# Performance work log

Measured on AMD Instinct MI355X. Metric: run time of the kernel, lower is better.

The kernel has to match this reference:

```python
import jax, jax.numpy as jnp
import numpy as np

COMMITMENT_COST = 0.25


def setup_inputs() -> dict:
    key = jax.random.key(0)
    k1, k2 = jax.random.split(key)
    B, S, D, K = 16, 4096, 256, 4096
    inputs = jax.random.normal(k1, (B, S, D), dtype=jnp.float32)
    # codebook ~ embedding.weight (init scale irrelevant for correctness baseline)
    codebook = jax.random.normal(k2, (K, D), dtype=jnp.float32)
    return {"inputs": inputs, "codebook": codebook}


def reference(inputs, codebook):
    B, S, D = inputs.shape
    flat = inputs.reshape(-1, D)  # (N, D)
    distances = (
        jnp.sum(flat * flat, axis=1, keepdims=True)
        + jnp.sum(codebook * codebook, axis=1)
        - 2.0 * jnp.matmul(flat, codebook.T)
    )
    encoding_indices = jnp.argmin(distances, axis=1)  # (N,)
    quantized = codebook[encoding_indices].reshape(inputs.shape)  # gather
    # commitment loss: beta * mse(inputs, sg(quantized))
    diff = inputs - jax.lax.stop_gradient(quantized)
    commitment_loss = COMMITMENT_COST * jnp.mean(diff * diff)
    # straight-through estimator
    quantized_st = inputs + jax.lax.stop_gradient(quantized - inputs)
    return quantized_st, commitment_loss, encoding_indices
```

## Files before the change

kernel.cpp:

```cpp
#include <hip/hip_runtime.h>
#include <stdint.h>

typedef _Float16 half8 __attribute__((ext_vector_type(8)));
typedef float f32x4 __attribute__((ext_vector_type(4)));

#define DDIM 256
#define KCODES 4096
#define BM 128
#define BN 128
#define DELTA 0.02f
#define FLT_BIG 3.4e38f

#define GLOAD_LDS(gsrc, ldst)                                                        \
    __builtin_amdgcn_global_load_lds(                                                \
        (const __attribute__((address_space(1))) void*)(const void*)(gsrc),          \
        (__attribute__((address_space(3))) void*)(void*)(ldst), 16, 0, 0)

__global__ void cvt_hl_kernel(const float* __restrict__ src, half8* __restrict__ dst) {
    int gid = blockIdx.x * 256 + threadIdx.x;
    int q = gid & 3;
    int ch = (gid >> 2) & 7;
    long row = gid >> 5;
    const float* s = src + row * DDIM + ch * 32 + q * 8;
    const float4 f0 = ((const float4*)s)[0];
    const float4 f1 = ((const float4*)s)[1];
    float vv[8] = {f0.x, f0.y, f0.z, f0.w, f1.x, f1.y, f1.z, f1.w};
    half8 hi, lo;
    #pragma unroll
    for (int j = 0; j < 8; ++j) {
        float v = vv[j];
        _Float16 h = (_Float16)v;
        hi[j] = h; lo[j] = (_Float16)(v - (float)h);
    }
    half8* d = dst + ((row * 8 + ch) << 3);
    d[q] = hi;
    d[q + 4] = lo;
}

__global__ void enorm_kernel(const float* __restrict__ cb, float* __restrict__ en, int K) {
    int gid = blockIdx.x * blockDim.x + threadIdx.x;
    int code = gid >> 6;
    int lane = threadIdx.x & 63;
    if (code >= K) return;
    const float4 v = *reinterpret_cast<const float4*>(&cb[(size_t)code * DDIM + lane * 4]);
    float s = v.x * v.x + v.y * v.y + v.z * v.z + v.w * v.w;
    #pragma unroll
    for (int off = 32; off > 0; off >>= 1) s += __shfl_xor(s, off, 64);
    if (lane == 0) en[code] = s;
}

__global__ __launch_bounds__(256, 2)
void vq_mfma_kernel(const half8* x16, const half8* __restrict__ cb16,
                    const float* __restrict__ en, int* __restrict__ bidx,
                    int* __restrict__ list, int* __restrict__ counter) {
    __shared__ __align__(16) half8 Abuf[2][BM * 8];
    __shared__ __align__(16) half8 Bbuf[2][BN * 8];
    __shared__ float red_d[2][BM];
    __shared__ float red_d2[2][BM];
    __shared__ int   red_i[2][BM];

    const int tid = threadIdx.x;
    const int lane = tid & 63;
    const int w = tid >> 6;
    const int wr = w >> 1, wc = w & 1;
    const int l15 = lane & 15, l4 = lane >> 4;
    const int brow = blockIdx.x * BM;

    const int lrow = lane >> 3;
    const int swz = (lane & 7) ^ lrow;
    const half8* pA0 = x16 + (size_t)(brow + (w     ) * 8 + lrow) * 64 + swz;
    const half8* pA1 = x16 + (size_t)(brow + (w +  4) * 8 + lrow) * 64 + swz;
    const half8* pA2 = x16 + (size_t)(brow + (w +  8) * 8 + lrow) * 64 + swz;
    const half8* pA3 = x16 + (size_t)(brow + (w + 12) * 8 + lrow) * 64 + swz;
    const half8* pB0 = cb16 + (size_t)((w     ) * 8 + lrow) * 64 + swz;
    const half8* pB1 = cb16 + (size_t)((w +  4) * 8 + lrow) * 64 + swz;
    const half8* pB2 = cb16 + (size_t)((w +  8) * 8 + lrow) * 64 + swz;
    const half8* pB3 = cb16 + (size_t)((w + 12) * 8 + lrow) * 64 + swz;

#define STAGE(b_) do {                                      \
        GLOAD_LDS(pA0, &Abuf[b_][(w     ) * 64]);           \
        GLOAD_LDS(pA1, &Abuf[b_][(w +  4) * 64]);           \
        GLOAD_LDS(pA2, &Abuf[b_][(w +  8) * 64]);           \
        GLOAD_LDS(pA3, &Abuf[b_][(w + 12) * 64]);           \
        GLOAD_LDS(pB0, &Bbuf[b_][(w     ) * 64]);           \
        GLOAD_LDS(pB1, &Bbuf[b_][(w +  4) * 64]);           \
        GLOAD_LDS(pB2, &Bbuf[b_][(w +  8) * 64]);           \
        GLOAD_LDS(pB3, &Bbuf[b_][(w + 12) * 64]);           \
    } while (0)

#define ADVA(dA_, dB_) do {                                 \
        pA0 += dA_; pA1 += dA_; pA2 += dA_; pA3 += dA_;     \
        pB0 += dB_; pB1 += dB_; pB2 += dB_; pB3 += dB_;     \
    } while (0)

    const int sw7 = l15 & 7;
    const _Float16* A0 = (const _Float16*)Abuf;
    const _Float16* B0 = A0 + 16384;
    const _Float16* aH = A0 + wr * 4096 + l15 * 64 + ((l4    ) ^ sw7) * 8;
    const _Float16* aL = A0 + wr * 4096 + l15 * 64 + ((l4 + 4) ^ sw7) * 8;
    const _Float16* bH = B0 + wc * 4096 + l15 * 64 + ((l4    ) ^ sw7) * 8;
    const _Float16* bL = B0 + wc * 4096 + l15 * 64 + ((l4 + 4) ^ sw7) * 8;

    STAGE(0); ADVA(8, 8);

    float bestv[4], best2v[4];
    int bidv[4];
    #pragma unroll
    for (int i = 0; i < 4; ++i) { bestv[i] = FLT_BIG; best2v[i] = FLT_BIG; bidv[i] = 0; }

    const int code_sub = wc * 64 + l4 * 4;
    f32x4 acc[4][4];

#define TRI(accr, bh_, bl_, ah_, al_) do {                                              \
        accr = __builtin_amdgcn_mfma_f32_16x16x32_f16(bh_, ah_, accr, 0, 0, 0);         \
        accr = __builtin_amdgcn_mfma_f32_16x16x32_f16(bl_, ah_, accr, 0, 0, 0);         \
        accr = __builtin_amdgcn_mfma_f32_16x16x32_f16(bh_, al_, accr, 0, 0, 0);         \
    } while (0)

    for (int it = 0; it < 32; ++it) {
        #pragma unroll
        for (int m = 0; m < 4; ++m)
            #pragma unroll
            for (int n = 0; n < 4; ++n) acc[m][n] = (f32x4){0.f, 0.f, 0.f, 0.f};

        #pragma unroll
        for (int k = 0; k < 8; ++k) {
            __syncthreads();
            if (k != 7) {
                STAGE((k + 1) & 1);
                if (k == 6) ADVA(-56, 8136);
                else        ADVA(8, 8);
            } else if (it != 31) {
                STAGE(0);
                ADVA(8, 8);
            }
            __builtin_amdgcn_sched_barrier(0);

            const int o = (k & 1) ? 8192 : 0;
            half8 ah[4], al[4], bh[4], bl[4];
            #pragma unroll
            for (int i = 0; i < 4; ++i) {
                ah[i] = *(const half8*)(aH + o + i * 1024);
                al[i] = *(const half8*)(aL + o + i * 1024);
                bh[i] = *(const half8*)(bH + o + i * 1024);
                bl[i] = *(const half8*)(bL + o + i * 1024);
            }
            __builtin_amdgcn_s_setprio(1);
            #pragma unroll
            for (int m = 0; m < 4; ++m)
                #pragma unroll
                for (int n = 0; n < 4; ++n)
                    TRI(acc[m][n], bh[m], bl[m], ah[n], al[n]);
            __builtin_amdgcn_s_setprio(0);
        }

        const int c0 = it * BN;
        #pragma unroll
        for (int m = 0; m < 4; ++m) {
            const float4 e4 = *(const float4*)(en + c0 + wc * 64 + m * 16 + l4 * 4);
            #pragma unroll
            for (int r = 0; r < 4; ++r) {
                int code = c0 + code_sub + m * 16 + r;
                float e = (r == 0) ? e4.x : (r == 1) ? e4.y : (r == 2) ? e4.z : e4.w;
                #pragma unroll
                for (int n = 0; n < 4; ++n) {
                    float dist = fmaf(-2.f, acc[m][n][r], e);
                    if (dist < bestv[n]) { best2v[n] = bestv[n]; bestv[n] = dist; bidv[n] = code; }
                    else if (dist < best2v[n]) best2v[n] = dist;
                }
            }
        }
    }
#undef STAGE
#undef ADVA
#undef TRI

    #pragma unroll
    for (int n = 0; n < 4; ++n) {
        float d = bestv[n], d2 = best2v[n];
        int ix = bidv[n];
        #pragma unroll
        for (int off = 16; off < 64; off <<= 1) {
            float od = __shfl_xor(d, off, 64);
            float od2 = __shfl_xor(d2, off, 64);
            int oi = __shfl_xor(ix, off, 64);
            if (od < d || (od == d && oi < ix)) { d2 = fminf(d, od2); d = od; ix = oi; }
            else d2 = fminf(d2, od);
        }
        if (l4 == 0) {
            int row = wr * 64 + n * 16 + l15;
            red_d[wc][row] = d;
            red_d2[wc][row] = d2;
            red_i[wc][row] = ix;
        }
    }
    __syncthreads();

    if (tid < BM) {
        float d = red_d[0][tid], d2 = red_d2[0][tid];
        int ix = red_i[0][tid];
        float od = red_d[1][tid], od2 = red_d2[1][tid];
        int oi = red_i[1][tid];
        if (od < d || (od == d && oi < ix)) { d2 = fminf(d, od2); d = od; ix = oi; }
        else d2 = fminf(d2, od);
        bidx[brow + tid] = ix;
        if (d2 - d < DELTA) {
            int pos = atomicAdd(counter, 1);
            list[pos] = brow + tid;
        }
    }
}

__global__ __launch_bounds__(256)
void rescan_kernel(const float* __restrict__ x, const float* __restrict__ cb,
                   const float* __restrict__ en, const int* __restrict__ list,
                   const int* __restrict__ counter, int* __restrict__ bidx) {
    __shared__ __align__(16) float4 xrow4[64];
    __shared__ float wd[4];
    __shared__ int wi[4];
    const int tid = threadIdx.x;
    const int w = tid >> 6;
    const int lane = tid & 63;
    const int cnt = *counter;

    for (int it = blockIdx.x; it < cnt; it += gridDim.x) {
        const int row = list[it];
        __syncthreads();
        if (tid < 64) xrow4[tid] = ((const float4*)&x[(size_t)row * DDIM])[tid];
        __syncthreads();
        const float4 xv = xrow4[lane];
        float bd = FLT_BIG;
        int bi = 0;
        for (int i = 0; i < KCODES / 4; ++i) {
            int code = i * 4 + w;
            const float4 c4 = ((const float4*)&cb[(size_t)code * DDIM])[lane];
            float s = xv.x * c4.x + xv.y * c4.y + xv.z * c4.z + xv.w * c4.w;
            #pragma unroll
            for (int off = 1; off < 64; off <<= 1) s += __shfl_xor(s, off, 64);
            float dist = fmaf(-2.f, s, en[code]);
            if (dist < bd) { bd = dist; bi = code; }
        }
        if (lane == 0) { wd[w] = bd; wi[w] = bi; }
        __syncthreads();
        if (tid == 0) {
            float d = wd[0]; int ix = wi[0];
            #pragma unroll
            for (int q = 1; q < 4; ++q) {
                if (wd[q] < d || (wd[q] == d && wi[q] < ix)) { d = wd[q]; ix = wi[q]; }
            }
            bidx[row] = ix;
        }
    }
}

__global__ __launch_bounds__(256)
void gather_kernel(const float* __restrict__ x, const float* __restrict__ cb,
                   const int* __restrict__ bidx, float* __restrict__ out,
                   float* __restrict__ loss_accum, int N) {
    __shared__ float wsum[4];
    __shared__ int bloc[64];
    const int tid = threadIdx.x;
    const int brow = blockIdx.x * 64;
    const size_t ND = (size_t)N * DDIM;
    if (tid < 64) {
        int ix = bidx[brow + tid];
        bloc[tid] = ix;
        out[ND + 1 + brow + tid] = (float)ix;
    }
    __syncthreads();
    float lsum = 0.f;
    #pragma unroll
    for (int pp = 0; pp < 16; ++pp) {
        int i = tid + pp * 256;
        int row = i >> 6;
        int c4 = (i & 63) << 2;
        int code = bloc[row];
        const float4 q = *reinterpret_cast<const float4*>(&cb[(size_t)code * DDIM + c4]);
        const float4 xv = *reinterpret_cast<const float4*>(&x[(size_t)(brow + row) * DDIM + c4]);
        float d0 = xv.x - q.x, d1 = xv.y - q.y, d2 = xv.z - q.z, d3 = xv.w - q.w;
        lsum += d0 * d0 + d1 * d1 + d2 * d2 + d3 * d3;
        *reinterpret_cast<float4*>(&out[(size_t)(brow + row) * DDIM + c4]) = q;
    }
    #pragma unroll
    for (int off = 32; off > 0; off >>= 1) lsum += __shfl_xor(lsum, off, 64);
    if ((tid & 63) == 0) wsum[tid >> 6] = lsum;
    __syncthreads();
    if (tid == 0) {
        float tot = wsum[0] + wsum[1] + wsum[2] + wsum[3];
        atomicAdd(loss_accum, tot * (0.25f / (float)ND));
    }
}

__global__ void loss_fin_kernel(const float* __restrict__ loss_accum,
                                float* __restrict__ out, size_t off) {
    if (blockIdx.x == 0 && threadIdx.x == 0) out[off] = *loss_accum;
}

extern "C" void kernel_launch(void* const* d_in, const int* in_sizes, int n_in,
                              void* d_out, int out_size, void* d_ws, size_t ws_size,
                              hipStream_t stream) {
    const float* x = (const float*)d_in[0];
    const float* cb = (const float*)d_in[1];
    const int N = in_sizes[0] / DDIM;
    const int K = in_sizes[1] / DDIM;
    float* out = (float*)d_out;

    half8* x16 = (half8*)d_out;

    half8* cb16 = (half8*)d_ws;
    char* p = (char*)d_ws + (4 << 20);
    float* en = (float*)p;                  p += (size_t)K * 4;
    int* bidx = (int*)p;                    p += (size_t)N * 4;
    int* list = (int*)p;                    p += (size_t)N * 4;
    int* counter = (int*)p;                 p += 64;
    float* loss_accum = (float*)p;

    hipMemsetAsync(counter, 0, sizeof(int), stream);
    hipMemsetAsync(loss_accum, 0, sizeof(float), stream);
    cvt_hl_kernel<<<(N * 32) / 256, 256, 0, stream>>>(x, x16);
    cvt_hl_kernel<<<(K * 32) / 256, 256, 0, stream>>>(cb, cb16);
    enorm_kernel<<<(K * 64) / 256, 256, 0, stream>>>(cb, en, K);
    vq_mfma_kernel<<<N / BM, 256, 0, stream>>>(x16, cb16, en, bidx, list, counter);
    rescan_kernel<<<512, 256, 0, stream>>>(x, cb, en, list, counter, bidx);
    gather_kernel<<<N / 64, 256, 0, stream>>>(x, cb, bidx, out, loss_accum, N);
    loss_fin_kernel<<<1, 64, 0, stream>>>(loss_accum, out, (size_t)N * DDIM);
}
```

Baseline: 727.2 us.

## Drop hi/lo split-fp16 and use plain fp16 MFMA with wider rescan margin

Converts inputs and codebook to a single fp16 copy instead of hi+lo pairs, which halves the staged data and the K-loop trip count. Each output tile now takes 2 MFMAs per 64-wide slice instead of 3 split-precision products. The candidate margin DELTA is raised from 0.02 to 0.10 to offset the lower-precision distances, so more rows get flagged for the exact fp32 rescan. This trades tensor-core and bandwidth work for possibly more rescan work.

```diff
diff --git a/kernel.cpp b/kernel.cpp
--- a/kernel.cpp
+++ b/kernel.cpp
@@ -8,7 +8,7 @@
 #define KCODES 4096
 #define BM 128
 #define BN 128
-#define DELTA 0.02f
+#define DELTA 0.10f
 #define FLT_BIG 3.4e38f
 
 #define GLOAD_LDS(gsrc, ldst)                                                        \
@@ -16,25 +16,19 @@
         (const __attribute__((address_space(1))) void*)(const void*)(gsrc),          \
         (__attribute__((address_space(3))) void*)(void*)(ldst), 16, 0, 0)
 
-__global__ void cvt_hl_kernel(const float* __restrict__ src, half8* __restrict__ dst) {
+__global__ void cvt_h_kernel(const float* __restrict__ src, half8* __restrict__ dst) {
     int gid = blockIdx.x * 256 + threadIdx.x;
-    int q = gid & 3;
-    int ch = (gid >> 2) & 7;
+    int s = gid & 31;
     long row = gid >> 5;
-    const float* s = src + row * DDIM + ch * 32 + q * 8;
-    const float4 f0 = ((const float4*)s)[0];
-    const float4 f1 = ((const float4*)s)[1];
-    float vv[8] = {f0.x, f0.y, f0.z, f0.w, f1.x, f1.y, f1.z, f1.w};
-    half8 hi, lo;
-    #pragma unroll
-    for (int j = 0; j < 8; ++j) {
-        float v = vv[j];
-        _Float16 h = (_Float16)v;
-        hi[j] = h; lo[j] = (_Float16)(v - (float)h);
-    }
-    half8* d = dst + ((row * 8 + ch) << 3);
-    d[q] = hi;
-    d[q + 4] = lo;
+    const float* p = src + row * DDIM + s * 8;
+    const float4 f0 = ((const float4*)p)[0];
+    const float4 f1 = ((const float4*)p)[1];
+    half8 h;
+    h[0] = (_Float16)f0.x; h[1] = (_Float16)f0.y;
+    h[2] = (_Float16)f0.z; h[3] = (_Float16)f0.w;
+    h[4] = (_Float16)f1.x; h[5] = (_Float16)f1.y;
+    h[6] = (_Float16)f1.z; h[7] = (_Float16)f1.w;
+    dst[gid] = h;
 }
 
 __global__ void enorm_kernel(const float* __restrict__ cb, float* __restrict__ en, int K) {
@@ -68,14 +62,14 @@
 
     const int lrow = lane >> 3;
     const int swz = (lane & 7) ^ lrow;
-    const half8* pA0 = x16 + (size_t)(brow + (w     ) * 8 + lrow) * 64 + swz;
-    const half8* pA1 = x16 + (size_t)(brow + (w +  4) * 8 + lrow) * 64 + swz;
-    const half8* pA2 = x16 + (size_t)(brow + (w +  8) * 8 + lrow) * 64 + swz;
-    const half8* pA3 = x16 + (size_t)(brow + (w + 12) * 8 + lrow) * 64 + swz;
-    const half8* pB0 = cb16 + (size_t)((w     ) * 8 + lrow) * 64 + swz;
-    const half8* pB1 = cb16 + (size_t)((w +  4) * 8 + lrow) * 64 + swz;
-    const half8* pB2 = cb16 + (size_t)((w +  8) * 8 + lrow) * 64 + swz;
-    const half8* pB3 = cb16 + (size_t)((w + 12) * 8 + lrow) * 64 + swz;
+    const half8* pA0 = x16 + (size_t)(brow + (w     ) * 8 + lrow) * 32 + swz;
+    const half8* pA1 = x16 + (size_t)(brow + (w +  4) * 8 + lrow) * 32 + swz;
+    const half8* pA2 = x16 + (size_t)(brow + (w +  8) * 8 + lrow) * 32 + swz;
+    const half8* pA3 = x16 + (size_t)(brow + (w + 12) * 8 + lrow) * 32 + swz;
+    const half8* pB0 = cb16 + (size_t)((w     ) * 8 + lrow) * 32 + swz;
+    const half8* pB1 = cb16 + (size_t)((w +  4) * 8 + lrow) * 32 + swz;
+    const half8* pB2 = cb16 + (size_t)((w +  8) * 8 + lrow) * 32 + swz;
+    const half8* pB3 = cb16 + (size_t)((w + 12) * 8 + lrow) * 32 + swz;
 
 #define STAGE(b_) do {                                      \
         GLOAD_LDS(pA0, &Abuf[b_][(w     ) * 64]);           \
@@ -94,12 +88,13 @@
     } while (0)
 
     const int sw7 = l15 & 7;
+    const int s0 = l4 ^ sw7;
     const _Float16* A0 = (const _Float16*)Abuf;
     const _Float16* B0 = A0 + 16384;
-    const _Float16* aH = A0 + wr * 4096 + l15 * 64 + ((l4    ) ^ sw7) * 8;
-    const _Float16* aL = A0 + wr * 4096 + l15 * 64 + ((l4 + 4) ^ sw7) * 8;
-    const _Float16* bH = B0 + wc * 4096 + l15 * 64 + ((l4    ) ^ sw7) * 8;
-    const _Float16* bL = B0 + wc * 4096 + l15 * 64 + ((l4 + 4) ^ sw7) * 8;
+    const _Float16* aH0 = A0 + (wr * 64 + l15) * 64 + s0 * 8;
+    const _Float16* aH1 = A0 + (wr * 64 + l15) * 64 + (s0 ^ 4) * 8;
+    const _Float16* bH0 = B0 + (wc * 64 + l15) * 64 + s0 * 8;
+    const _Float16* bH1 = B0 + (wc * 64 + l15) * 64 + (s0 ^ 4) * 8;
 
     STAGE(0); ADVA(8, 8);
 
@@ -110,12 +105,6 @@
 
     const int code_sub = wc * 64 + l4 * 4;
     f32x4 acc[4][4];
-
-#define TRI(accr, bh_, bl_, ah_, al_) do {                                              \
-        accr = __builtin_amdgcn_mfma_f32_16x16x32_f16(bh_, ah_, accr, 0, 0, 0);         \
-        accr = __builtin_amdgcn_mfma_f32_16x16x32_f16(bl_, ah_, accr, 0, 0, 0);         \
-        accr = __builtin_amdgcn_mfma_f32_16x16x32_f16(bh_, al_, accr, 0, 0, 0);         \
-    } while (0)
 
     for (int it = 0; it < 32; ++it) {
         #pragma unroll
@@ -124,11 +113,11 @@
             for (int n = 0; n < 4; ++n) acc[m][n] = (f32x4){0.f, 0.f, 0.f, 0.f};
 
         #pragma unroll
-        for (int k = 0; k < 8; ++k) {
+        for (int k = 0; k < 4; ++k) {
             __syncthreads();
-            if (k != 7) {
+            if (k != 3) {
                 STAGE((k + 1) & 1);
-                if (k == 6) ADVA(-56, 8136);
+                if (k == 2) ADVA(-24, 4072);
                 else        ADVA(8, 8);
             } else if (it != 31) {
                 STAGE(0);
@@ -137,20 +126,22 @@
             __builtin_amdgcn_sched_barrier(0);
 
             const int o = (k & 1) ? 8192 : 0;
-            half8 ah[4], al[4], bh[4], bl[4];
+            half8 a0[4], a1[4], b0[4], b1[4];
             #pragma unroll
             for (int i = 0; i < 4; ++i) {
-                ah[i] = *(const half8*)(aH + o + i * 1024);
-                al[i] = *(const half8*)(aL + o + i * 1024);
-                bh[i] = *(const half8*)(bH + o + i * 1024);
-                bl[i] = *(const half8*)(bL + o + i * 1024);
+                a0[i] = *(const half8*)(aH0 + o + i * 1024);
+                a1[i] = *(const half8*)(aH1 + o + i * 1024);
+                b0[i] = *(const half8*)(bH0 + o + i * 1024);
+                b1[i] = *(const half8*)(bH1 + o + i * 1024);
             }
             __builtin_amdgcn_s_setprio(1);
             #pragma unroll
             for (int m = 0; m < 4; ++m)
                 #pragma unroll
-                for (int n = 0; n < 4; ++n)
-                    TRI(acc[m][n], bh[m], bl[m], ah[n], al[n]);
+                for (int n = 0; n < 4; ++n) {
+                    acc[m][n] = __builtin_amdgcn_mfma_f32_16x16x32_f16(b0[m], a0[n], acc[m][n], 0, 0, 0);
+                    acc[m][n] = __builtin_amdgcn_mfma_f32_16x16x32_f16(b1[m], a1[n], acc[m][n], 0, 0, 0);
+                }
             __builtin_amdgcn_s_setprio(0);
         }
 
@@ -173,7 +164,6 @@
     }
 #undef STAGE
 #undef ADVA
-#undef TRI
 
     #pragma unroll
     for (int n = 0; n < 4; ++n) {
@@ -308,7 +298,7 @@
     half8* x16 = (half8*)d_out;
 
     half8* cb16 = (half8*)d_ws;
-    char* p = (char*)d_ws + (4 << 20);
+    char* p = (char*)d_ws + (2 << 20);
     float* en = (float*)p;                  p += (size_t)K * 4;
     int* bidx = (int*)p;                    p += (size_t)N * 4;
     int* list = (int*)p;                    p += (size_t)N * 4;
@@ -317,8 +307,8 @@
 
     hipMemsetAsync(counter, 0, sizeof(int), stream);
     hipMemsetAsync(loss_accum, 0, sizeof(float), stream);
-    cvt_hl_kernel<<<(N * 32) / 256, 256, 0, stream>>>(x, x16);
-    cvt_hl_kernel<<<(K * 32) / 256, 256, 0, stream>>>(cb, cb16);
+    cvt_h_kernel<<<(N * 32) / 256, 256, 0, stream>>>(x, x16);
+    cvt_h_kernel<<<(K * 32) / 256, 256, 0, stream>>>(cb, cb16);
     enorm_kernel<<<(K * 64) / 256, 256, 0, stream>>>(cb, en, K);
     vq_mfma_kernel<<<N / BM, 256, 0, stream>>>(x16, cb16, en, bidx, list, counter);
     rescan_kernel<<<512, 256, 0, stream>>>(x, cb, en, list, counter, bidx);
```

New measurement: 756.0 us. 4.0% more time.
